# Performance work log

Measured on AMD Instinct MI355X. Metric: run time of the kernel, lower is better.

The kernel has to match this reference:

```python
import jax, jax.numpy as jnp
import numpy as np

N, T, C, U, H = 256, 128, 64, 512, 256


def _gru_step(h, x, Wg, bg, Wc, bc):
    # TF GRUCell: r,u = sigmoid([x,h] @ Wg + bg); c = tanh([x, r*h] @ Wc + bc)
    # new_h = u * h + (1 - u) * c   (bg initialized to 1.0 in TF)
    ru = jax.nn.sigmoid(jnp.concatenate([x, h], axis=-1) @ Wg + bg)
    r, u = jnp.split(ru, 2, axis=-1)
    c = jnp.tanh(jnp.concatenate([x, r * h], axis=-1) @ Wc + bc)
    return u * h + (1.0 - u) * c


def setup_inputs() -> dict:
    key = jax.random.key(0)
    ks = jax.random.split(key, 8)
    s = lambda fan_in: 1.0 / np.sqrt(fan_in)
    return {
        "frames": jax.random.normal(ks[0], (N, T, C), jnp.float32),
        "Wg1": jax.random.normal(ks[1], (C + U, 2 * U), jnp.float32) * s(C + U),
        "bg1": jnp.ones((2 * U,), jnp.float32),
        "Wc1": jax.random.normal(ks[2], (C + U, U), jnp.float32) * s(C + U),
        "bc1": jnp.zeros((U,), jnp.float32),
        "Wg2": jax.random.normal(ks[3], (2 * U, 2 * U), jnp.float32) * s(2 * U),
        "bg2": jnp.ones((2 * U,), jnp.float32),
        "Wc2": jax.random.normal(ks[4], (2 * U, U), jnp.float32) * s(2 * U),
        "bc2": jnp.zeros((U,), jnp.float32),
        "Wh": jax.random.normal(ks[5], (U, H), jnp.float32) * s(U),
        "bh": jnp.zeros((H,), jnp.float32),
        "Wp": jax.random.normal(ks[6], (H, C), jnp.float32) * s(H),
        "bp": jnp.zeros((C,), jnp.float32),
    }


def reference(frames, Wg1, bg1, Wc1, bc1, Wg2, bg2, Wc2, bc2, Wh, bh, Wp, bp):
    n = frames.shape[0]
    xs = jnp.swapaxes(frames, 0, 1)  # [T, N, C] time-major for scan

    def step(carry, x_t):
        h1, h2 = carry
        h1 = _gru_step(h1, x_t, Wg1, bg1, Wc1, bc1)
        h2 = _gru_step(h2, h1, Wg2, bg2, Wc2, bc2)
        return (h1, h2), h2

    h0 = (jnp.zeros((n, U), frames.dtype), jnp.zeros((n, U), frames.dtype))
    _, ys = jax.lax.scan(step, h0, xs)  # ys: [T, N, U]
    outputs = jnp.swapaxes(ys, 0, 1)  # [N, T, U] (use_cell_state=False)
    hidden = jax.nn.elu(outputs @ Wh + bh)  # dense0, ELU
    predicted = hidden @ Wp + bp  # predict_1: linear back to sensor_count
    return predicted
```

## Files before the change

### kernel.cpp

```cpp
#include <hip/hip_runtime.h>
#include <cstdint>
#include <cstddef>


#define NWG 256
#define TPB 512

constexpr int N_ = 256, T_ = 128, C_ = 64, U_ = 512, H_ = 256;

typedef __attribute__((ext_vector_type(8))) short short8;
typedef __attribute__((ext_vector_type(4))) float f32x4;

constexpr size_t HPB      = 262144;
constexpr size_t OFF_HP   = 16384;
constexpr size_t OFF_RH1  = OFF_HP + 8 * HPB;
constexpr size_t OFF_RH2  = OFF_RH1 + 524288;
constexpr size_t OFF_G1U  = OFF_RH2 + 524288;
constexpr size_t OFF_G2U  = OFF_G1U + 524288;
constexpr size_t OFF_HID  = OFF_G2U + 524288;
constexpr size_t OFF_XHI  = OFF_HID + 262144;
constexpr size_t OFF_XLO  = OFF_XHI + 4194304;
constexpr size_t OFF_WG1S = OFF_XLO + 4194304;
constexpr size_t OFF_WC1S = OFF_WG1S + 32 * 81920;
constexpr size_t OFF_WG2S = OFF_WC1S + 32 * 40960;
constexpr size_t OFF_WC2S = OFF_WG2S + 32 * 131072;
constexpr size_t OFF_WHS  = OFF_WC2S + 32 * 65536;
constexpr size_t OFF_WPS  = OFF_WHS + 16 * 32768;
constexpr size_t WS_NEED  = OFF_WPS + 4 * 16384;

__device__ __forceinline__ float sigmoidf_(float z) {
  return 1.0f / (1.0f + __expf(-z));
}
__device__ __forceinline__ float tanhf_(float z) {
  return 1.0f - 2.0f / (1.0f + __expf(2.0f * z));
}
__device__ __forceinline__ unsigned short bf_hi(float f) {
  unsigned int x = __float_as_uint(f);
  unsigned int r = x + 0x7FFFu + ((x >> 16) & 1u);
  return (unsigned short)(r >> 16);
}
__device__ __forceinline__ float bf_f(unsigned v) {
  return __uint_as_float((v & 0xFFFFu) << 16);
}
__device__ __forceinline__ float bf_fh(unsigned v) {
  return __uint_as_float(v & 0xFFFF0000u);
}
__device__ __forceinline__ unsigned short bf_lo(float f, unsigned short hi) {
  return bf_hi(f - __uint_as_float(((unsigned)hi) << 16));
}

__device__ void writeStream(const float* __restrict__ W, int ldW, int colbase,
                            char* sb, int nsplit, int slots, int tnn, int nch) {
  const int tid = threadIdx.x;
  const int lane = tid & 63;
  const int e = tid >> 6;
  const int nf = nsplit * slots * tnn;
  for (int f = 0; f < nf; ++f) {
    int tn = f % tnn;
    int ci = (f / tnn) % slots;
    int ks = f / (tnn * slots);
    int c = ks + ci * nsplit;
    int k = 32 * c + ((lane >> 4) << 3) + e;
    int col = colbase + 16 * tn + (lane & 15);
    float v = (c < nch) ? W[(size_t)k * ldW + col] : 0.f;
    unsigned short hi = bf_hi(v);
    unsigned short lo = bf_lo(v, hi);
    unsigned short* fb = (unsigned short*)(sb + (size_t)f * 2048);
    fb[lane * 8 + e] = hi;
    fb[512 + lane * 8 + e] = lo;
  }
}

template <int TM, int TN, int NSPLIT, int SLOTS, int KA>
__device__ __forceinline__ void mm_core(
    const unsigned short* __restrict__ A1h, const unsigned short* __restrict__ A1l,
    int lda1, int aoff,
    const unsigned short* __restrict__ A2h, const unsigned short* __restrict__ A2l,
    int lda2, const char* __restrict__ bstr, float* red, int row0loc) {
  const int tid = threadIdx.x;
  const int ww = tid >> 6, lane = tid & 63;
  const int tm = ww / NSPLIT;
  const int ks = ww % NSPLIT;
  const int arow = row0loc + 16 * tm + (lane & 15);
  const int kgrp = (lane >> 4) << 3;

  uint4 Ah[SLOTS], Al[SLOTS];
#pragma unroll
  for (int ci = 0; ci < SLOTS; ++ci) {
    const int c = ks + ci * NSPLIT;
    const int ak = 32 * c + kgrp;
    const unsigned short *ph, *pl;
    if (ak < KA) {
      ph = A1h + (size_t)arow * lda1 + aoff + ak;
      pl = A1l + (size_t)arow * lda1 + aoff + ak;
    } else {
      const int ak2 = ak - KA;
      ph = A2h + (size_t)arow * lda2 + ak2;
      pl = A2l + (size_t)arow * lda2 + ak2;
    }
    Ah[ci] = *(const uint4*)ph;
    Al[ci] = *(const uint4*)pl;
  }

  f32x4 acc0[TN], acc1[TN], acc2[TN];
#pragma unroll
  for (int tn = 0; tn < TN; ++tn) {
    acc0[tn] = (f32x4){0.f, 0.f, 0.f, 0.f};
    acc1[tn] = (f32x4){0.f, 0.f, 0.f, 0.f};
    acc2[tn] = (f32x4){0.f, 0.f, 0.f, 0.f};
  }
#pragma unroll
  for (int ci = 0; ci < SLOTS; ++ci) {
    union { uint4 u; short8 s; } ah, al;
    ah.u = Ah[ci]; al.u = Al[ci];
    const char* fb = bstr + ((size_t)(ks * SLOTS + ci) * TN) * 2048;
#pragma unroll
    for (int tn = 0; tn < TN; ++tn) {
      union { uint4 u; short8 s; } bh, bl;
      bh.u = *(const uint4*)((const unsigned short*)(fb + (size_t)tn * 2048) + lane * 8);
      bl.u = *(const uint4*)((const unsigned short*)(fb + (size_t)tn * 2048 + 1024) + lane * 8);
      acc0[tn] = __builtin_amdgcn_mfma_f32_16x16x32_bf16(ah.s, bh.s, acc0[tn], 0, 0, 0);
      acc1[tn] = __builtin_amdgcn_mfma_f32_16x16x32_bf16(ah.s, bl.s, acc1[tn], 0, 0, 0);
      acc2[tn] = __builtin_amdgcn_mfma_f32_16x16x32_bf16(al.s, bh.s, acc2[tn], 0, 0, 0);
    }
  }
#pragma unroll
  for (int tn = 0; tn < TN; ++tn) {
    f32x4 s = acc0[tn] + acc1[tn] + acc2[tn];
    int slot = (tm * TN + tn) * NSPLIT + ks;
    *(f32x4*)(&red[slot * 256 + lane * 4]) = s;
  }
}

template <int TM, int TN, int NSPLIT, typename F>
__device__ __forceinline__ void epi2(const float* red, int row0loc, int col0, F f) {
  for (int idx = threadIdx.x; idx < TM * TN * 128; idx += TPB) {
    int tg = idx >> 7;
    int r  = (idx >> 3) & 15;
    int cp = idx & 7;
    int e0 = (((((r >> 2) << 4) | (cp << 1)) << 2) | (r & 3));
    float z0 = 0.f, z1 = 0.f;
#pragma unroll
    for (int s = 0; s < NSPLIT; ++s) {
      const float* rp = red + (tg * NSPLIT + s) * 256;
      z0 += rp[e0];
      z1 += rp[e0 + 4];
    }
    int tm = tg / TN, tn = tg % TN;
    f(row0loc + 16 * tm + r, col0 + 16 * tn + cp * 2, z0, z1);
  }
}

struct Ptrs {
  unsigned short *xhi, *xlo, *rh1hi, *rh1lo, *rh2hi, *rh2lo, *hidhi, *hidlo;
  float *g1u, *g2u;
};
__device__ __forceinline__ Ptrs mkptrs(char* wsb) {
  Ptrs p;
  p.xhi = (unsigned short*)(wsb + OFF_XHI);
  p.xlo = (unsigned short*)(wsb + OFF_XLO);
  p.rh1hi = (unsigned short*)(wsb + OFF_RH1);
  p.rh1lo = (unsigned short*)(wsb + OFF_RH1 + 262144);
  p.rh2hi = (unsigned short*)(wsb + OFF_RH2);
  p.rh2lo = (unsigned short*)(wsb + OFF_RH2 + 262144);
  p.hidhi = (unsigned short*)(wsb + OFF_HID);
  p.hidlo = (unsigned short*)(wsb + OFF_HID + 131072);
  p.g1u = (float*)(wsb + OFF_G1U);
  p.g2u = (float*)(wsb + OFF_G2U);
  return p;
}
__device__ __forceinline__ unsigned short* hplane(char* wsb, int parity) {
  return (unsigned short*)(wsb + OFF_HP + (size_t)parity * 4 * HPB);
}

__device__ __forceinline__ void p1_body(char* wsb, const float* __restrict__ bg1,
                                        int ts, int m, int n, float* red) {
  const int row0 = m * 32;
  const int ps = ts & 1;
  Ptrs pp = mkptrs(wsb);
  unsigned short* h1hi_p = hplane(wsb, ps);
  unsigned short* h1lo_p = h1hi_p + 131072;
  const char* wg1s = (const char*)(wsb + OFF_WG1S + (size_t)n * 81920);
  mm_core<2, 2, 4, 5, 64>(pp.xhi, pp.xlo, 8192, ts * 64, h1hi_p, h1lo_p, 512,
                          wg1s, red, row0);
  __syncthreads();
  epi2<2, 2, 4>(red, row0, n * 32, [&](int row, int col, float z0, float z1) {
    z0 += bg1[col]; z1 += bg1[col + 1];
    float s0 = sigmoidf_(z0), s1 = sigmoidf_(z1);
    if (col < 512) {
      size_t ix = (size_t)row * 512 + col;
      unsigned hw = *(const unsigned*)(h1hi_p + ix);
      unsigned lw = *(const unsigned*)(h1lo_p + ix);
      float h0 = bf_f(hw) + bf_f(lw);
      float h1v = bf_fh(hw) + bf_fh(lw);
      float r0 = s0 * h0, r1 = s1 * h1v;
      unsigned short a0 = bf_hi(r0), a1 = bf_hi(r1);
      *(unsigned*)(pp.rh1hi + ix) = (unsigned)a0 | ((unsigned)a1 << 16);
      *(unsigned*)(pp.rh1lo + ix) = (unsigned)bf_lo(r0, a0) | ((unsigned)bf_lo(r1, a1) << 16);
    } else {
      float2 g = {s0, s1};
      *(float2*)(pp.g1u + (size_t)row * 512 + (col - 512)) = g;
    }
  });
}

extern "C" __global__ __launch_bounds__(TPB, 2)
void k_prolog(const float* __restrict__ frames,
              const float* __restrict__ Wg1, const float* __restrict__ Wc1,
              const float* __restrict__ Wg2, const float* __restrict__ Wc2,
              const float* __restrict__ Wh, const float* __restrict__ Wp,
              char* __restrict__ wsb) {
  const int tid = threadIdx.x;
  const int wg = blockIdx.x;
  unsigned short* xhi = (unsigned short*)(wsb + OFF_XHI);
  unsigned short* xlo = (unsigned short*)(wsb + OFF_XLO);
  const size_t base = (size_t)wg * 8192;
  for (int i = tid; i < 8192; i += TPB) {
    float v = frames[base + i];
    unsigned short h = bf_hi(v);
    xhi[base + i] = h;
    xlo[base + i] = bf_lo(v, h);
  }
  if (wg < 32) {
    writeStream(Wg1, 1024, wg * 32, wsb + OFF_WG1S + (size_t)wg * 81920, 4, 5, 2, 18);
    writeStream(Wc1, 512, wg * 16, wsb + OFF_WC1S + (size_t)wg * 40960, 4, 5, 1, 18);
    writeStream(Wg2, 1024, wg * 32, wsb + OFF_WG2S + (size_t)wg * 131072, 4, 8, 2, 32);
    writeStream(Wc2, 512, wg * 16, wsb + OFF_WC2S + (size_t)wg * 65536, 4, 8, 1, 32);
  }
  if (wg < 16) writeStream(Wh, 256, wg * 16, wsb + OFF_WHS + (size_t)wg * 32768, 8, 2, 1, 16);
  if (wg < 4)  writeStream(Wp, 64, wg * 16, wsb + OFF_WPS + (size_t)wg * 16384, 8, 1, 1, 8);
}

extern "C" __global__ __launch_bounds__(TPB, 2)
void k_p1(char* __restrict__ wsb, const float* __restrict__ bg1, int t) {
  __shared__ float red[4096];
  const int wg = blockIdx.x;
  p1_body(wsb, bg1, t, wg >> 5, wg & 31, red);
}

extern "C" __global__ __launch_bounds__(TPB, 2)
void k_s1(char* __restrict__ wsb, const float* __restrict__ bc1,
          const float* __restrict__ bh, int t) {
  __shared__ float red[4096];
  const int wg = blockIdx.x;
  const int m = wg >> 5, n = wg & 31;
  const int row0 = m * 32;
  const int p = t & 1, q = p ^ 1;
  Ptrs pp = mkptrs(wsb);
  unsigned short* h1hi_p = hplane(wsb, p);
  unsigned short* h1lo_p = h1hi_p + 131072;
  unsigned short* h2hi_p = h1hi_p + 262144;
  unsigned short* h2lo_p = h1hi_p + 393216;
  unsigned short* h1hi_q = hplane(wsb, q);
  unsigned short* h1lo_q = h1hi_q + 131072;
  const char* wc1s = (const char*)(wsb + OFF_WC1S + (size_t)n * 40960);
  const int b2 = n & 15, a2 = n >> 4;
  const char* whs = (const char*)(wsb + OFF_WHS + (size_t)b2 * 32768);

  if (t < T_)
    mm_core<2, 1, 4, 5, 64>(pp.xhi, pp.xlo, 8192, t * 64, pp.rh1hi, pp.rh1lo, 512,
                            wc1s, red, row0);
  if (t > 0)
    mm_core<1, 1, 8, 2, 512>(h2hi_p, h2lo_p, 512, 0, nullptr, nullptr, 0,
                             whs, red + 2048, row0 + 16 * a2);
  __syncthreads();
  if (t < T_) {
    epi2<2, 1, 4>(red, row0, n * 16, [&](int row, int col, float z0, float z1) {
      z0 += bc1[col]; z1 += bc1[col + 1];
      float c0 = tanhf_(z0), c1 = tanhf_(z1);
      size_t ix = (size_t)row * 512 + col;
      float2 ug = *(const float2*)(pp.g1u + ix);
      unsigned hw = *(const unsigned*)(h1hi_p + ix);
      unsigned lw = *(const unsigned*)(h1lo_p + ix);
      float h0 = bf_f(hw) + bf_f(lw);
      float h1v = bf_fh(hw) + bf_fh(lw);
      float n0 = ug.x * h0 + (1.f - ug.x) * c0;
      float n1 = ug.y * h1v + (1.f - ug.y) * c1;
      unsigned short a0 = bf_hi(n0), a1 = bf_hi(n1);
      *(unsigned*)(h1hi_q + ix) = (unsigned)a0 | ((unsigned)a1 << 16);
      *(unsigned*)(h1lo_q + ix) = (unsigned)bf_lo(n0, a0) | ((unsigned)bf_lo(n1, a1) << 16);
    });
  }
  if (t > 0) {
    epi2<1, 1, 8>(red + 2048, row0 + 16 * a2, 16 * b2,
                  [&](int row, int col, float z0, float z1) {
      z0 += bh[col]; z1 += bh[col + 1];
      float e0v = z0 > 0.f ? z0 : __expf(z0) - 1.f;
      float e1v = z1 > 0.f ? z1 : __expf(z1) - 1.f;
      size_t ix = (size_t)row * 256 + col;
      unsigned short a0 = bf_hi(e0v), a1 = bf_hi(e1v);
      *(unsigned*)(pp.hidhi + ix) = (unsigned)a0 | ((unsigned)a1 << 16);
      *(unsigned*)(pp.hidlo + ix) = (unsigned)bf_lo(e0v, a0) | ((unsigned)bf_lo(e1v, a1) << 16);
    });
  }
}

extern "C" __global__ __launch_bounds__(TPB, 2)
void k_s2(char* __restrict__ wsb, const float* __restrict__ bg2,
          const float* __restrict__ bp, float* __restrict__ out, int t) {
  __shared__ float red[6144];
  const int wg = blockIdx.x;
  const int m = wg >> 5, n = wg & 31;
  const int row0 = m * 32;
  const int p = t & 1, q = p ^ 1;
  Ptrs pp = mkptrs(wsb);
  unsigned short* h1hi_p = hplane(wsb, p);
  unsigned short* h2hi_p = h1hi_p + 262144;
  unsigned short* h2lo_p = h1hi_p + 393216;
  unsigned short* h1hi_q = hplane(wsb, q);
  unsigned short* h1lo_q = h1hi_q + 131072;
  const char* wg2s = (const char*)(wsb + OFF_WG2S + (size_t)n * 131072);
  const int b4 = n & 3, a4 = (n >> 2) & 1;
  const char* wps = (const char*)(wsb + OFF_WPS + (size_t)b4 * 16384);

  if (t < T_)
    mm_core<2, 2, 4, 8, 512>(h1hi_q, h1lo_q, 512, 0, h2hi_p, h2lo_p, 512,
                             wg2s, red, row0);
  if (t > 0 && n < 8)
    mm_core<1, 1, 8, 1, 256>(pp.hidhi, pp.hidlo, 256, 0, nullptr, nullptr, 0,
                             wps, red + 4096, row0 + 16 * a4);
  __syncthreads();
  if (t < T_) {
    epi2<2, 2, 4>(red, row0, n * 32, [&](int row, int col, float z0, float z1) {
      z0 += bg2[col]; z1 += bg2[col + 1];
      float s0 = sigmoidf_(z0), s1 = sigmoidf_(z1);
      if (col < 512) {
        size_t ix = (size_t)row * 512 + col;
        unsigned hw = *(const unsigned*)(h2hi_p + ix);
        unsigned lw = *(const unsigned*)(h2lo_p + ix);
        float h0 = bf_f(hw) + bf_f(lw);
        float h1v = bf_fh(hw) + bf_fh(lw);
        float r0 = s0 * h0, r1 = s1 * h1v;
        unsigned short a0 = bf_hi(r0), a1 = bf_hi(r1);
        *(unsigned*)(pp.rh2hi + ix) = (unsigned)a0 | ((unsigned)a1 << 16);
        *(unsigned*)(pp.rh2lo + ix) = (unsigned)bf_lo(r0, a0) | ((unsigned)bf_lo(r1, a1) << 16);
      } else {
        float2 g = {s0, s1};
        *(float2*)(pp.g2u + (size_t)row * 512 + (col - 512)) = g;
      }
    });
  }
  if (t > 0 && n < 8) {
    epi2<1, 1, 8>(red + 4096, row0 + 16 * a4, 16 * b4,
                  [&](int row, int col, float z0, float z1) {
      float2 v = {z0 + bp[col], z1 + bp[col + 1]};
      *(float2*)(out + (size_t)row * 8192 + (size_t)(t - 1) * 64 + col) = v;
    });
  }
}

extern "C" __global__ __launch_bounds__(TPB, 2)
void k_s3(char* __restrict__ wsb, const float* __restrict__ bc2,
          const float* __restrict__ bg1, int t) {
  __shared__ float red[6144];
  const int wg = blockIdx.x;
  const int m = wg >> 5, n = wg & 31;
  const int row0 = m * 32;
  const int p = t & 1, q = p ^ 1;
  Ptrs pp = mkptrs(wsb);
  unsigned short* h1hi_p = hplane(wsb, p);
  unsigned short* h2hi_p = h1hi_p + 262144;
  unsigned short* h2lo_p = h1hi_p + 393216;
  unsigned short* h1hi_q = hplane(wsb, q);
  unsigned short* h1lo_q = h1hi_q + 131072;
  unsigned short* h2hi_q = h1hi_q + 262144;
  unsigned short* h2lo_q = h1hi_q + 393216;
  const char* wc2s = (const char*)(wsb + OFF_WC2S + (size_t)n * 65536);

  mm_core<2, 1, 4, 8, 512>(h1hi_q, h1lo_q, 512, 0, pp.rh2hi, pp.rh2lo, 512,
                           wc2s, red, row0);
  __syncthreads();
  epi2<2, 1, 4>(red, row0, n * 16, [&](int row, int col, float z0, float z1) {
    z0 += bc2[col]; z1 += bc2[col + 1];
    float c0 = tanhf_(z0), c1 = tanhf_(z1);
    size_t ix = (size_t)row * 512 + col;
    float2 ug = *(const float2*)(pp.g2u + ix);
    unsigned hw = *(const unsigned*)(h2hi_p + ix);
    unsigned lw = *(const unsigned*)(h2lo_p + ix);
    float h0 = bf_f(hw) + bf_f(lw);
    float h1v = bf_fh(hw) + bf_fh(lw);
    float n0 = ug.x * h0 + (1.f - ug.x) * c0;
    float n1 = ug.y * h1v + (1.f - ug.y) * c1;
    unsigned short a0 = bf_hi(n0), a1 = bf_hi(n1);
    *(unsigned*)(h2hi_q + ix) = (unsigned)a0 | ((unsigned)a1 << 16);
    *(unsigned*)(h2lo_q + ix) = (unsigned)bf_lo(n0, a0) | ((unsigned)bf_lo(n1, a1) << 16);
  });
  if (t + 1 < T_) {
    __syncthreads();
    p1_body(wsb, bg1, t + 1, m, n, red + 2048);
  }
}

constexpr size_t F_SZ_H   = (size_t)N_ * U_;
constexpr size_t F_OFF_H1 = 0;
constexpr size_t F_OFF_H2 = F_OFF_H1 + 2 * F_SZ_H;
constexpr size_t F_OFF_BAR = F_OFF_H2 + 2 * F_SZ_H;
constexpr size_t F_OFF_G1 = F_OFF_BAR + 64;
constexpr size_t F_OFF_G2 = F_OFF_G1 + (size_t)N_ * 1024;
constexpr size_t F_OFF_HID = F_OFF_G2 + (size_t)N_ * 1024;
constexpr int LDP = 257;

__device__ __forceinline__ void gbarF(unsigned* b, unsigned np) {
  __syncthreads();
  if (threadIdx.x == 0) {
    __threadfence();
    unsigned e = __hip_atomic_load(b + 16, __ATOMIC_RELAXED, __HIP_MEMORY_SCOPE_AGENT);
    unsigned a = __hip_atomic_fetch_add(b, 1u, __ATOMIC_ACQ_REL, __HIP_MEMORY_SCOPE_AGENT);
    if (a == np - 1) {
      __hip_atomic_store(b, 0u, __ATOMIC_RELAXED, __HIP_MEMORY_SCOPE_AGENT);
      __hip_atomic_store(b + 16, e + 1u, __ATOMIC_RELEASE, __HIP_MEMORY_SCOPE_AGENT);
    } else {
      unsigned spins = 0;
      while (__hip_atomic_load(b + 16, __ATOMIC_RELAXED, __HIP_MEMORY_SCOPE_AGENT) == e) {
        __builtin_amdgcn_s_sleep(1);
        if (++spins > (1u << 20)) break;
      }
    }
    __threadfence();
  }
  __syncthreads();
}

template <int CK, bool GATED>
__device__ __forceinline__ void stage(float (*lds)[LDP],
                                      const float* __restrict__ src, int sStride, int sOff,
                                      const float* __restrict__ gate, int gStride, int gOff,
                                      int row0) {
  constexpr int PER = CK / 16;
  const int r = threadIdx.x >> 4;
  const int c0 = (threadIdx.x & 15) * PER;
  const float* s = src + (size_t)(row0 + r) * sStride + sOff + c0;
  float4 a0, a1, a2, a3;
  a0 = *(const float4*)(s);
  if constexpr (PER >= 8) a1 = *(const float4*)(s + 4);
  if constexpr (PER >= 16) { a2 = *(const float4*)(s + 8); a3 = *(const float4*)(s + 12); }
  if constexpr (GATED) {
    const float* g = gate + (size_t)(row0 + r) * gStride + gOff + c0;
    float4 g0 = *(const float4*)(g);
    a0.x *= g0.x; a0.y *= g0.y; a0.z *= g0.z; a0.w *= g0.w;
    if constexpr (PER >= 8) {
      float4 g1v = *(const float4*)(g + 4);
      a1.x *= g1v.x; a1.y *= g1v.y; a1.z *= g1v.z; a1.w *= g1v.w;
    }
    if constexpr (PER >= 16) {
      float4 g2v = *(const float4*)(g + 8);
      float4 g3v = *(const float4*)(g + 12);
      a2.x *= g2v.x; a2.y *= g2v.y; a2.z *= g2v.z; a2.w *= g2v.w;
      a3.x *= g3v.x; a3.y *= g3v.y; a3.z *= g3v.z; a3.w *= g3v.w;
    }
  }
  float* d = &lds[r][c0];
  d[0] = a0.x; d[1] = a0.y; d[2] = a0.z; d[3] = a0.w;
  if constexpr (PER >= 8) { d[4] = a1.x; d[5] = a1.y; d[6] = a1.z; d[7] = a1.w; }
  if constexpr (PER >= 16) {
    d[8] = a2.x; d[9] = a2.y; d[10] = a2.z; d[11] = a2.w;
    d[12] = a3.x; d[13] = a3.y; d[14] = a3.z; d[15] = a3.w;
  }
}
template <int CK>
__device__ __forceinline__ void fma2(float2& acc, const float (*lds)[LDP], int row,
                                     const float* __restrict__ B, int ldB) {
#pragma unroll 8
  for (int k = 0; k < CK; ++k) {
    const float a = lds[row][k];
    const float2 b = *(const float2*)(B + (size_t)k * ldB);
    acc.x = fmaf(a, b.x, acc.x);
    acc.y = fmaf(a, b.y, acc.y);
  }
}
template <int CK>
__device__ __forceinline__ void fma1(float& acc, const float (*lds)[LDP], int row,
                                     const float* __restrict__ B, int ldB) {
#pragma unroll 8
  for (int k = 0; k < CK; ++k) acc = fmaf(lds[row][k], B[(size_t)k * ldB], acc);
}

extern "C" __global__ __launch_bounds__(TPB, 2)
void gru_persistent(const float* __restrict__ frames,
                    const float* __restrict__ Wg1, const float* __restrict__ bg1,
                    const float* __restrict__ Wc1, const float* __restrict__ bc1,
                    const float* __restrict__ Wg2, const float* __restrict__ bg2,
                    const float* __restrict__ Wc2, const float* __restrict__ bc2,
                    const float* __restrict__ Wh,  const float* __restrict__ bh,
                    const float* __restrict__ Wp,  const float* __restrict__ bp,
                    float* __restrict__ out, float* __restrict__ ws) {
  __shared__ float lds[32][LDP];
  float* h1b = ws + F_OFF_H1;
  float* h2b = ws + F_OFF_H2;
  unsigned* bar = (unsigned*)(ws + F_OFF_BAR);
  float* g1 = ws + F_OFF_G1;
  float* g2 = ws + F_OFF_G2;
  float* hid = ws + F_OFF_HID;
  const int tid = threadIdx.x;
  const int wg = blockIdx.x;
  const int xcd = wg & 7, grp = wg >> 3;
  const int m_blk = grp >> 2, n_blk = (xcd << 2) | (grp & 3);
  const int row0 = m_blk * 32;
  const int rowA = tid & 31, cq = tid >> 5;
  const int nrow = row0 + rowA;
  for (int t = 0; t <= T_; ++t) {
    const int p = t & 1;
    const float* h1o = h1b + (size_t)p * F_SZ_H;
    float* h1n = h1b + (size_t)(p ^ 1) * F_SZ_H;
    const float* h2o = h2b + (size_t)p * F_SZ_H;
    float* h2n = h2b + (size_t)(p ^ 1) * F_SZ_H;
    if (t < T_) {
      float2 acc = {0.f, 0.f};
      const int col = n_blk * 32 + cq * 2;
      stage<64, false>(lds, frames, T_ * C_, t * C_, nullptr, 0, 0, row0);
      __syncthreads();
      fma2<64>(acc, lds, rowA, Wg1 + col, 1024);
      __syncthreads();
#pragma unroll 1
      for (int ch = 0; ch < 2; ++ch) {
        stage<256, false>(lds, h1o, U_, ch * 256, nullptr, 0, 0, row0);
        __syncthreads();
        fma2<256>(acc, lds, rowA, Wg1 + (size_t)(64 + ch * 256) * 1024 + col, 1024);
        __syncthreads();
      }
      const float2 bb = *(const float2*)(bg1 + col);
      float* gp = g1 + (size_t)nrow * 1024 + col;
      gp[0] = sigmoidf_(acc.x + bb.x);
      gp[1] = sigmoidf_(acc.y + bb.y);
    }
    gbarF(bar, NWG);
    if (t < T_) {
      float acc = 0.f;
      const int col = n_blk * 16 + cq;
      stage<64, false>(lds, frames, T_ * C_, t * C_, nullptr, 0, 0, row0);
      __syncthreads();
      fma1<64>(acc, lds, rowA, Wc1 + col, U_);
      __syncthreads();
#pragma unroll 1
      for (int ch = 0; ch < 2; ++ch) {
        stage<256, true>(lds, h1o, U_, ch * 256, g1, 1024, ch * 256, row0);
        __syncthreads();
        fma1<256>(acc, lds, rowA, Wc1 + (size_t)(64 + ch * 256) * U_ + col, U_);
        __syncthreads();
      }
      const float cv = tanhf_(acc + bc1[col]);
      const float u = g1[(size_t)nrow * 1024 + 512 + col];
      const float ho = h1o[(size_t)nrow * U_ + col];
      h1n[(size_t)nrow * U_ + col] = u * ho + (1.f - u) * cv;
    }
    if (t > 0) {
      float acc = 0.f;
      const int col = n_blk * 8 + (cq & 7);
      const bool act = tid < 256;
#pragma unroll 1
      for (int ch = 0; ch < 2; ++ch) {
        stage<256, false>(lds, h2o, U_, ch * 256, nullptr, 0, 0, row0);
        __syncthreads();
        if (act) fma1<256>(acc, lds, rowA, Wh + (size_t)(ch * 256) * H_ + col, H_);
        __syncthreads();
      }
      if (act) {
        const float z = acc + bh[col];
        hid[(size_t)nrow * H_ + col] = z > 0.f ? z : __expf(z) - 1.f;
      }
    }
    gbarF(bar, NWG);
    if (t < T_) {
      float2 acc = {0.f, 0.f};
      const int col = n_blk * 32 + cq * 2;
#pragma unroll 1
      for (int ch = 0; ch < 4; ++ch) {
        const float* src = (ch < 2) ? h1n : h2o;
        stage<256, false>(lds, src, U_, (ch & 1) * 256, nullptr, 0, 0, row0);
        __syncthreads();
        fma2<256>(acc, lds, rowA, Wg2 + (size_t)(ch * 256) * 1024 + col, 1024);
        __syncthreads();
      }
      const float2 bb = *(const float2*)(bg2 + col);
      float* gp = g2 + (size_t)nrow * 1024 + col;
      gp[0] = sigmoidf_(acc.x + bb.x);
      gp[1] = sigmoidf_(acc.y + bb.y);
    }
    gbarF(bar, NWG);
    if (t < T_) {
      float acc = 0.f;
      const int col = n_blk * 16 + cq;
#pragma unroll 1
      for (int ch = 0; ch < 4; ++ch) {
        if (ch < 2) stage<256, false>(lds, h1n, U_, (ch & 1) * 256, nullptr, 0, 0, row0);
        else stage<256, true>(lds, h2o, U_, (ch & 1) * 256, g2, 1024, (ch & 1) * 256, row0);
        __syncthreads();
        fma1<256>(acc, lds, rowA, Wc2 + (size_t)(ch * 256) * U_ + col, U_);
        __syncthreads();
      }
      const float cv = tanhf_(acc + bc2[col]);
      const float u = g2[(size_t)nrow * 1024 + 512 + col];
      const float ho = h2o[(size_t)nrow * U_ + col];
      h2n[(size_t)nrow * U_ + col] = u * ho + (1.f - u) * cv;
    }
    if (t > 0) {
      if (tid < 64) {
        float acc = 0.f;
        const int col = n_blk * 2 + cq;
        const float* hrow = hid + (size_t)nrow * H_;
#pragma unroll 8
        for (int k = 0; k < H_; ++k) acc = fmaf(hrow[k], Wp[(size_t)k * C_ + col], acc);
        out[(size_t)nrow * (T_ * C_) + (size_t)(t - 1) * C_ + col] = acc + bp[col];
      }
    }
  }
}

extern "C" void kernel_launch(void* const* d_in, const int* in_sizes, int n_in,
                              void* d_out, int out_size, void* d_ws, size_t ws_size,
                              hipStream_t stream) {
  const float* frames = (const float*)d_in[0];
  const float* Wg1 = (const float*)d_in[1];
  const float* bg1 = (const float*)d_in[2];
  const float* Wc1 = (const float*)d_in[3];
  const float* bc1 = (const float*)d_in[4];
  const float* Wg2 = (const float*)d_in[5];
  const float* bg2 = (const float*)d_in[6];
  const float* Wc2 = (const float*)d_in[7];
  const float* bc2 = (const float*)d_in[8];
  const float* Wh = (const float*)d_in[9];
  const float* bh = (const float*)d_in[10];
  const float* Wp = (const float*)d_in[11];
  const float* bp = (const float*)d_in[12];
  float* out = (float*)d_out;

  if (ws_size >= WS_NEED) {
    char* wsb = (char*)d_ws;
    hipMemsetAsync(d_ws, 0, 16384 + 4 * HPB, stream);
    hipLaunchKernelGGL(k_prolog, dim3(NWG), dim3(TPB), 0, stream,
                       frames, Wg1, Wc1, Wg2, Wc2, Wh, Wp, wsb);
    hipLaunchKernelGGL(k_p1, dim3(NWG), dim3(TPB), 0, stream, wsb, bg1, 0);
    for (int t = 0; t <= T_; ++t) {
      hipLaunchKernelGGL(k_s1, dim3(NWG), dim3(TPB), 0, stream, wsb, bc1, bh, t);
      hipLaunchKernelGGL(k_s2, dim3(NWG), dim3(TPB), 0, stream, wsb, bg2, bp, out, t);
      if (t < T_)
        hipLaunchKernelGGL(k_s3, dim3(NWG), dim3(TPB), 0, stream, wsb, bc2, bg1, t);
    }
  } else {
    float* ws = (float*)d_ws;
    hipMemsetAsync(d_ws, 0, F_OFF_G1 * sizeof(float), stream);
    void* args[] = {(void*)&frames, (void*)&Wg1, (void*)&bg1, (void*)&Wc1, (void*)&bc1,
                    (void*)&Wg2, (void*)&bg2, (void*)&Wc2, (void*)&bc2,
                    (void*)&Wh, (void*)&bh, (void*)&Wp, (void*)&bp,
                    (void*)&out, (void*)&ws};
    hipError_t err = hipLaunchCooperativeKernel((const void*)gru_persistent,
                                                dim3(NWG), dim3(TPB), args, 0, stream);
    if (err != hipSuccess) {
      (void)hipGetLastError();
      hipLaunchKernelGGL(gru_persistent, dim3(NWG), dim3(TPB), 0, stream,
                         frames, Wg1, bg1, Wc1, bc1, Wg2, bg2, Wc2, bc2,
                         Wh, bh, Wp, bp, out, ws);
    }
  }
}
```

Measured before the change: 3.776 ms.

## Double grid to 512 workgroups with 16-row tiles and wider K split

Each per-step kernel now launches 512 workgroups, each handling 16 batch rows instead of 32. The K dimension is split across 8 wave groups instead of 4, with fewer chunks per group, and the pre-swizzled weight streams are re-laid out to match. The dense-head and projection tiles are remapped to use fewer workgroups. The goal is more parallelism per step on the latency-bound recurrent chain, at the cost of each weight slice being read by twice as many workgroups and more cross-wave reduction. p1_body is also marked noinline.

```diff
diff --git a/kernel.cpp b/kernel.cpp
--- a/kernel.cpp
+++ b/kernel.cpp
@@ -21,8 +21,8 @@
 constexpr size_t OFF_XHI  = OFF_HID + 262144;
 constexpr size_t OFF_XLO  = OFF_XHI + 4194304;
 constexpr size_t OFF_WG1S = OFF_XLO + 4194304;
-constexpr size_t OFF_WC1S = OFF_WG1S + 32 * 81920;
-constexpr size_t OFF_WG2S = OFF_WC1S + 32 * 40960;
+constexpr size_t OFF_WC1S = OFF_WG1S + 32 * 98304;
+constexpr size_t OFF_WG2S = OFF_WC1S + 32 * 49152;
 constexpr size_t OFF_WC2S = OFF_WG2S + 32 * 131072;
 constexpr size_t OFF_WHS  = OFF_WC2S + 32 * 65536;
 constexpr size_t OFF_WPS  = OFF_WHS + 16 * 32768;
@@ -173,18 +173,19 @@
   return (unsigned short*)(wsb + OFF_HP + (size_t)parity * 4 * HPB);
 }
 
-__device__ __forceinline__ void p1_body(char* wsb, const float* __restrict__ bg1,
-                                        int ts, int m, int n, float* red) {
-  const int row0 = m * 32;
+__device__ __attribute__((noinline)) void p1_body(char* wsb,
+                                                  const float* __restrict__ bg1,
+                                                  int ts, int n, int row0loc,
+                                                  float* red) {
   const int ps = ts & 1;
   Ptrs pp = mkptrs(wsb);
   unsigned short* h1hi_p = hplane(wsb, ps);
   unsigned short* h1lo_p = h1hi_p + 131072;
-  const char* wg1s = (const char*)(wsb + OFF_WG1S + (size_t)n * 81920);
-  mm_core<2, 2, 4, 5, 64>(pp.xhi, pp.xlo, 8192, ts * 64, h1hi_p, h1lo_p, 512,
-                          wg1s, red, row0);
+  const char* wg1s = (const char*)(wsb + OFF_WG1S + (size_t)n * 98304);
+  mm_core<1, 2, 8, 3, 64>(pp.xhi, pp.xlo, 8192, ts * 64, h1hi_p, h1lo_p, 512,
+                          wg1s, red, row0loc);
   __syncthreads();
-  epi2<2, 2, 4>(red, row0, n * 32, [&](int row, int col, float z0, float z1) {
+  epi2<1, 2, 8>(red, row0loc, n * 32, [&](int row, int col, float z0, float z1) {
     z0 += bg1[col]; z1 += bg1[col + 1];
     float s0 = sigmoidf_(z0), s1 = sigmoidf_(z1);
     if (col < 512) {
@@ -222,10 +223,10 @@
     xlo[base + i] = bf_lo(v, h);
   }
   if (wg < 32) {
-    writeStream(Wg1, 1024, wg * 32, wsb + OFF_WG1S + (size_t)wg * 81920, 4, 5, 2, 18);
-    writeStream(Wc1, 512, wg * 16, wsb + OFF_WC1S + (size_t)wg * 40960, 4, 5, 1, 18);
-    writeStream(Wg2, 1024, wg * 32, wsb + OFF_WG2S + (size_t)wg * 131072, 4, 8, 2, 32);
-    writeStream(Wc2, 512, wg * 16, wsb + OFF_WC2S + (size_t)wg * 65536, 4, 8, 1, 32);
+    writeStream(Wg1, 1024, wg * 32, wsb + OFF_WG1S + (size_t)wg * 98304, 8, 3, 2, 18);
+    writeStream(Wc1, 512, wg * 16, wsb + OFF_WC1S + (size_t)wg * 49152, 8, 3, 1, 18);
+    writeStream(Wg2, 1024, wg * 32, wsb + OFF_WG2S + (size_t)wg * 131072, 8, 4, 2, 32);
+    writeStream(Wc2, 512, wg * 16, wsb + OFF_WC2S + (size_t)wg * 65536, 8, 4, 1, 32);
   }
   if (wg < 16) writeStream(Wh, 256, wg * 16, wsb + OFF_WHS + (size_t)wg * 32768, 8, 2, 1, 16);
   if (wg < 4)  writeStream(Wp, 64, wg * 16, wsb + OFF_WPS + (size_t)wg * 16384, 8, 1, 1, 8);
@@ -235,7 +236,8 @@
 void k_p1(char* __restrict__ wsb, const float* __restrict__ bg1, int t) {
   __shared__ float red[4096];
   const int wg = blockIdx.x;
-  p1_body(wsb, bg1, t, wg >> 5, wg & 31, red);
+  const int n = wg & 31, hh = (wg >> 5) & 1, m = wg >> 6;
+  p1_body(wsb, bg1, t, n, m * 32 + 16 * hh, red);
 }
 
 extern "C" __global__ __launch_bounds__(TPB, 2)
@@ -243,8 +245,8 @@
           const float* __restrict__ bh, int t) {
   __shared__ float red[4096];
   const int wg = blockIdx.x;
-  const int m = wg >> 5, n = wg & 31;
-  const int row0 = m * 32;
+  const int n = wg & 31, hh = (wg >> 5) & 1, m = wg >> 6;
+  const int row0loc = m * 32 + 16 * hh;
   const int p = t & 1, q = p ^ 1;
   Ptrs pp = mkptrs(wsb);
   unsigned short* h1hi_p = hplane(wsb, p);
@@ -253,19 +255,18 @@
   unsigned short* h2lo_p = h1hi_p + 393216;
   unsigned short* h1hi_q = hplane(wsb, q);
   unsigned short* h1lo_q = h1hi_q + 131072;
-  const char* wc1s = (const char*)(wsb + OFF_WC1S + (size_t)n * 40960);
-  const int b2 = n & 15, a2 = n >> 4;
-  const char* whs = (const char*)(wsb + OFF_WHS + (size_t)b2 * 32768);
+  const char* wc1s = (const char*)(wsb + OFF_WC1S + (size_t)n * 49152);
+  const char* whs = (const char*)(wsb + OFF_WHS + (size_t)n * 32768);
 
   if (t < T_)
-    mm_core<2, 1, 4, 5, 64>(pp.xhi, pp.xlo, 8192, t * 64, pp.rh1hi, pp.rh1lo, 512,
-                            wc1s, red, row0);
-  if (t > 0)
+    mm_core<1, 1, 8, 3, 64>(pp.xhi, pp.xlo, 8192, t * 64, pp.rh1hi, pp.rh1lo, 512,
+                            wc1s, red, row0loc);
+  if (t > 0 && n < 16)
     mm_core<1, 1, 8, 2, 512>(h2hi_p, h2lo_p, 512, 0, nullptr, nullptr, 0,
-                             whs, red + 2048, row0 + 16 * a2);
+                             whs, red + 2048, row0loc);
   __syncthreads();
   if (t < T_) {
-    epi2<2, 1, 4>(red, row0, n * 16, [&](int row, int col, float z0, float z1) {
+    epi2<1, 1, 8>(red, row0loc, n * 16, [&](int row, int col, float z0, float z1) {
       z0 += bc1[col]; z1 += bc1[col + 1];
       float c0 = tanhf_(z0), c1 = tanhf_(z1);
       size_t ix = (size_t)row * 512 + col;
@@ -281,8 +282,8 @@
       *(unsigned*)(h1lo_q + ix) = (unsigned)bf_lo(n0, a0) | ((unsigned)bf_lo(n1, a1) << 16);
     });
   }
-  if (t > 0) {
-    epi2<1, 1, 8>(red + 2048, row0 + 16 * a2, 16 * b2,
+  if (t > 0 && n < 16) {
+    epi2<1, 1, 8>(red + 2048, row0loc, 16 * n,
                   [&](int row, int col, float z0, float z1) {
       z0 += bh[col]; z1 += bh[col + 1];
       float e0v = z0 > 0.f ? z0 : __expf(z0) - 1.f;
@@ -300,8 +301,8 @@
           const float* __restrict__ bp, float* __restrict__ out, int t) {
   __shared__ float red[6144];
   const int wg = blockIdx.x;
-  const int m = wg >> 5, n = wg & 31;
-  const int row0 = m * 32;
+  const int n = wg & 31, hh = (wg >> 5) & 1, m = wg >> 6;
+  const int row0loc = m * 32 + 16 * hh;
   const int p = t & 1, q = p ^ 1;
   Ptrs pp = mkptrs(wsb);
   unsigned short* h1hi_p = hplane(wsb, p);
@@ -310,18 +311,17 @@
   unsigned short* h1hi_q = hplane(wsb, q);
   unsigned short* h1lo_q = h1hi_q + 131072;
   const char* wg2s = (const char*)(wsb + OFF_WG2S + (size_t)n * 131072);
-  const int b4 = n & 3, a4 = (n >> 2) & 1;
-  const char* wps = (const char*)(wsb + OFF_WPS + (size_t)b4 * 16384);
+  const char* wps = (const char*)(wsb + OFF_WPS + (size_t)n * 16384);
 
   if (t < T_)
-    mm_core<2, 2, 4, 8, 512>(h1hi_q, h1lo_q, 512, 0, h2hi_p, h2lo_p, 512,
-                             wg2s, red, row0);
-  if (t > 0 && n < 8)
+    mm_core<1, 2, 8, 4, 512>(h1hi_q, h1lo_q, 512, 0, h2hi_p, h2lo_p, 512,
+                             wg2s, red, row0loc);
+  if (t > 0 && n < 4)
     mm_core<1, 1, 8, 1, 256>(pp.hidhi, pp.hidlo, 256, 0, nullptr, nullptr, 0,
-                             wps, red + 4096, row0 + 16 * a4);
+                             wps, red + 4096, row0loc);
   __syncthreads();
   if (t < T_) {
-    epi2<2, 2, 4>(red, row0, n * 32, [&](int row, int col, float z0, float z1) {
+    epi2<1, 2, 8>(red, row0loc, n * 32, [&](int row, int col, float z0, float z1) {
       z0 += bg2[col]; z1 += bg2[col + 1];
       float s0 = sigmoidf_(z0), s1 = sigmoidf_(z1);
       if (col < 512) {
@@ -340,8 +340,8 @@
       }
     });
   }
-  if (t > 0 && n < 8) {
-    epi2<1, 1, 8>(red + 4096, row0 + 16 * a4, 16 * b4,
+  if (t > 0 && n < 4) {
+    epi2<1, 1, 8>(red + 4096, row0loc, 16 * n,
                   [&](int row, int col, float z0, float z1) {
       float2 v = {z0 + bp[col], z1 + bp[col + 1]};
       *(float2*)(out + (size_t)row * 8192 + (size_t)(t - 1) * 64 + col) = v;
@@ -354,8 +354,8 @@
           const float* __restrict__ bg1, int t) {
   __shared__ float red[6144];
   const int wg = blockIdx.x;
-  const int m = wg >> 5, n = wg & 31;
-  const int row0 = m * 32;
+  const int n = wg & 31, hh = (wg >> 5) & 1, m = wg >> 6;
+  const int row0loc = m * 32 + 16 * hh;
   const int p = t & 1, q = p ^ 1;
   Ptrs pp = mkptrs(wsb);
   unsigned short* h1hi_p = hplane(wsb, p);
@@ -367,10 +367,10 @@
   unsigned short* h2lo_q = h1hi_q + 393216;
   const char* wc2s = (const char*)(wsb + OFF_WC2S + (size_t)n * 65536);
 
-  mm_core<2, 1, 4, 8, 512>(h1hi_q, h1lo_q, 512, 0, pp.rh2hi, pp.rh2lo, 512,
-                           wc2s, red, row0);
+  mm_core<1, 1, 8, 4, 512>(h1hi_q, h1lo_q, 512, 0, pp.rh2hi, pp.rh2lo, 512,
+                           wc2s, red, row0loc);
   __syncthreads();
-  epi2<2, 1, 4>(red, row0, n * 16, [&](int row, int col, float z0, float z1) {
+  epi2<1, 1, 8>(red, row0loc, n * 16, [&](int row, int col, float z0, float z1) {
     z0 += bc2[col]; z1 += bc2[col + 1];
     float c0 = tanhf_(z0), c1 = tanhf_(z1);
     size_t ix = (size_t)row * 512 + col;
@@ -387,7 +387,7 @@
   });
   if (t + 1 < T_) {
     __syncthreads();
-    p1_body(wsb, bg1, t + 1, m, n, red + 2048);
+    p1_body(wsb, bg1, t + 1, n, row0loc, red + 2048);
   }
 }
 
@@ -629,12 +629,12 @@
     hipMemsetAsync(d_ws, 0, 16384 + 4 * HPB, stream);
     hipLaunchKernelGGL(k_prolog, dim3(NWG), dim3(TPB), 0, stream,
                        frames, Wg1, Wc1, Wg2, Wc2, Wh, Wp, wsb);
-    hipLaunchKernelGGL(k_p1, dim3(NWG), dim3(TPB), 0, stream, wsb, bg1, 0);
+    hipLaunchKernelGGL(k_p1, dim3(512), dim3(TPB), 0, stream, wsb, bg1, 0);
     for (int t = 0; t <= T_; ++t) {
-      hipLaunchKernelGGL(k_s1, dim3(NWG), dim3(TPB), 0, stream, wsb, bc1, bh, t);
-      hipLaunchKernelGGL(k_s2, dim3(NWG), dim3(TPB), 0, stream, wsb, bg2, bp, out, t);
+      hipLaunchKernelGGL(k_s1, dim3(512), dim3(TPB), 0, stream, wsb, bc1, bh, t);
+      hipLaunchKernelGGL(k_s2, dim3(512), dim3(TPB), 0, stream, wsb, bg2, bp, out, t);
       if (t < T_)
-        hipLaunchKernelGGL(k_s3, dim3(NWG), dim3(TPB), 0, stream, wsb, bc2, bg1, t);
+        hipLaunchKernelGGL(k_s3, dim3(512), dim3(TPB), 0, stream, wsb, bc2, bg1, t);
     }
   } else {
     float* ws = (float*)d_ws;
```

Result: slower. 3.937 ms (+4.2%).
